# Performance work log

Hardware: AMD Instinct MI355X
Metric: run time of the kernel (lower is better)

Reference implementation:

```python
import jax, jax.numpy as jnp
import numpy as np

N_NODES = 100000
N_EDGES = 1600000
D_FEAT = 64
ORDER = 2


def setup_inputs() -> dict:
    key = jax.random.key(0)
    k1, k2, k3, k4 = jax.random.split(key, 4)
    x = jax.random.normal(k1, (N_NODES, D_FEAT), dtype=jnp.float32)
    edge_row = jnp.sort(jax.random.randint(k2, (N_EDGES,), 0, N_NODES, dtype=jnp.int32))
    edge_col = jax.random.randint(k3, (N_EDGES,), 0, N_NODES, dtype=jnp.int32)
    # positive edge weights ~ normalized adjacency values
    edge_val = jax.random.uniform(k4, (N_EDGES,), dtype=jnp.float32)
    return {"x": x, "edge_row": edge_row, "edge_col": edge_col, "edge_val": edge_val}


def reference(x, edge_row, edge_col, edge_val):
    # SGConvolution: x <- adj @ x, repeated `order` times (no trainable params).
    # adj is sparse COO: adj[edge_row[e], edge_col[e]] = edge_val[e].
    def spmm(h):
        # gather source features, scale by edge weight, scatter-add to rows
        msg = edge_val[:, None] * h[edge_col]          # [E, D]
        return jax.ops.segment_sum(msg, edge_row, num_segments=N_NODES)  # [N, D]

    h = x
    for _ in range(ORDER):
        h = spmm(h)
    return h
```

## Files before the change

### kernel.cpp

```cpp
#include <hip/hip_runtime.h>
#include <hip/hip_fp16.h>


#define N_NODES 100000
#define N_EDGES 1600000
#define D_FEAT  64
#define EPW     64
#define CH      16

#define N_ELEM   (N_NODES * D_FEAT)
#define N_CAST   (N_ELEM / 4)
#define N_Z16    (N_ELEM / 8)
#define N_ZOUT   (N_ELEM / 4)
#define PREP_TASKS (N_CAST + N_Z16 + N_ZOUT)

__device__ __forceinline__ float readlane_f(float x, int j) {
    return __uint_as_float(__builtin_amdgcn_readlane(__float_as_uint(x), j));
}

template <bool HALF_OUT>
__device__ __forceinline__ void flush(void* outp, int row, int lane, float acc) {
    if constexpr (HALF_OUT) {
        const float partner = __shfl_xor(acc, 1);
        if ((lane & 1) == 0) {
            __half2* o = (__half2*)outp;
            unsafeAtomicAdd(&o[(size_t)row * (D_FEAT / 2) + (lane >> 1)],
                            __floats2half2_rn(acc, partner));
        }
    } else {
        atomicAdd(&((float*)outp)[(size_t)row * D_FEAT + lane], acc);
    }
}

template <bool HALF_OUT>
__global__ __launch_bounds__(256) void sg_spmm(
    const __half* __restrict__ h,
    const int*    __restrict__ erow,
    const int*    __restrict__ ecol,
    const float*  __restrict__ eval,
    void*         __restrict__ outp)
{
    const int lane  = threadIdx.x & 63;
    const int wave  = (int)((blockIdx.x * blockDim.x + threadIdx.x) >> 6);
    const int start = wave * EPW;

    const int   r_v = erow[start + lane];
    const int   c_v = ecol[start + lane];
    const float w_v = eval[start + lane];

    __half gbuf[2][CH];

#pragma unroll
    for (int j = 0; j < CH; ++j) {
        const int c = __builtin_amdgcn_readlane(c_v, j);
        gbuf[0][j] = h[(size_t)c * D_FEAT + lane];
    }

    int   cur_row = __builtin_amdgcn_readlane(r_v, 0);
    float acc     = 0.0f;

#pragma unroll
    for (int k = 0; k < EPW / CH; ++k) {
        if (k + 1 < EPW / CH) {
#pragma unroll
            for (int j = 0; j < CH; ++j) {
                const int c = __builtin_amdgcn_readlane(c_v, (k + 1) * CH + j);
                gbuf[(k + 1) & 1][j] = h[(size_t)c * D_FEAT + lane];
            }
        }
#pragma unroll
        for (int j = 0; j < CH; ++j) {
            const int e = k * CH + j;
            const int r = __builtin_amdgcn_readlane(r_v, e);
            if (r != cur_row) {
                flush<HALF_OUT>(outp, cur_row, lane, acc);
                acc = 0.0f;
                cur_row = r;
            }
            acc += readlane_f(w_v, e) * __half2float(gbuf[k & 1][j]);
        }
    }
    flush<HALF_OUT>(outp, cur_row, lane, acc);
}

__global__ __launch_bounds__(256) void prep(
    const float* __restrict__ x,
    __half*      __restrict__ h16a,
    __half*      __restrict__ h16b,
    float*       __restrict__ out)
{
    const int i = blockIdx.x * blockDim.x + threadIdx.x;
    if (i < N_CAST) {
        const float4 v = ((const float4*)x)[i];
        const __half2 a = __floats2half2_rn(v.x, v.y);
        const __half2 b = __floats2half2_rn(v.z, v.w);
        uint2 u;
        u.x = *(const unsigned int*)&a;
        u.y = *(const unsigned int*)&b;
        ((uint2*)h16a)[i] = u;
    } else if (i < N_CAST + N_Z16) {
        ((uint4*)h16b)[i - N_CAST] = make_uint4(0u, 0u, 0u, 0u);
    } else {
        ((float4*)out)[i - (N_CAST + N_Z16)] = make_float4(0.f, 0.f, 0.f, 0.f);
    }
}

extern "C" void kernel_launch(void* const* d_in, const int* in_sizes, int n_in,
                              void* d_out, int out_size, void* d_ws, size_t ws_size,
                              hipStream_t stream) {
    const float* x    = (const float*)d_in[0];
    const int*   erow = (const int*)  d_in[1];
    const int*   ecol = (const int*)  d_in[2];
    const float* eval = (const float*)d_in[3];
    float*       out  = (float*)d_out;

    __half* h16a = (__half*)d_ws;
    __half* h16b = h16a + N_ELEM;

    const int threads     = 256;
    const int prep_blocks = PREP_TASKS / threads;
    const int spmm_blocks = (N_EDGES / EPW) * 64 / threads;

    prep<<<prep_blocks, threads, 0, stream>>>(x, h16a, h16b, out);
    sg_spmm<true ><<<spmm_blocks, threads, 0, stream>>>(h16a, erow, ecol, eval, h16b);
    sg_spmm<false><<<spmm_blocks, threads, 0, stream>>>(h16b, erow, ecol, eval, out);
}
```

Baseline: 153.9 us.

## Split each wave into half-waves that gather half2 rows over 32 edges

The SpMM kernel now splits each 64-lane wave into two 32-lane halves. Each half processes 32 of the wave's edges, and each lane loads a 4-byte half2 (two features) per edge instead of a single 2-byte half. Edge indices, rows and weights are broadcast with ds_bpermute instead of readlane, and all 32 gathers are issued up front rather than in double-buffered chunks of 16. This is meant to halve the load count per lane, widen each access and expose more memory-level parallelism. In exchange it costs more registers, a now-divergent per-half flush branch, and extra shuffles to re-order the fp32 output atomics.

After: 157.9 us. 1.03x slower.

```diff
diff --git a/kernel.cpp b/kernel.cpp
--- a/kernel.cpp
+++ b/kernel.cpp
@@ -6,7 +6,6 @@
 #define N_EDGES 1600000
 #define D_FEAT  64
 #define EPW     64
-#define CH      16
 
 #define N_ELEM   (N_NODES * D_FEAT)
 #define N_CAST   (N_ELEM / 4)
@@ -14,22 +13,35 @@
 #define N_ZOUT   (N_ELEM / 4)
 #define PREP_TASKS (N_CAST + N_Z16 + N_ZOUT)
 
-__device__ __forceinline__ float readlane_f(float x, int j) {
-    return __uint_as_float(__builtin_amdgcn_readlane(__float_as_uint(x), j));
+__device__ __forceinline__ int bperm(int baddr, int off, int v) {
+    return __builtin_amdgcn_ds_bpermute(baddr + off, v);
+}
+
+__device__ __forceinline__ void flush_f32(float* o, int row, int lane,
+                                          float ax, float ay) {
+    const int m = lane & 31;
+    const int H = lane & 32;
+    const float sx = __shfl(ax, H + (m >> 1));
+    const float sy = __shfl(ay, H + (m >> 1));
+    const float tx = __shfl(ax, H + 16 + (m >> 1));
+    const float ty = __shfl(ay, H + 16 + (m >> 1));
+    const float vA = (m & 1) ? sy : sx;
+    const float vB = (m & 1) ? ty : tx;
+    atomicAdd(&o[(size_t)row * D_FEAT + m], vA);
+    atomicAdd(&o[(size_t)row * D_FEAT + 32 + m], vB);
 }
 
 template <bool HALF_OUT>
-__device__ __forceinline__ void flush(void* outp, int row, int lane, float acc) {
+__device__ __forceinline__ void flush(void* outp, int row, int lane,
+                                      float& ax, float& ay) {
     if constexpr (HALF_OUT) {
-        const float partner = __shfl_xor(acc, 1);
-        if ((lane & 1) == 0) {
-            __half2* o = (__half2*)outp;
-            unsafeAtomicAdd(&o[(size_t)row * (D_FEAT / 2) + (lane >> 1)],
-                            __floats2half2_rn(acc, partner));
-        }
+        __half2* o = (__half2*)outp;
+        unsafeAtomicAdd(&o[(size_t)row * (D_FEAT / 2) + (lane & 31)],
+                        __floats2half2_rn(ax, ay));
     } else {
-        atomicAdd(&((float*)outp)[(size_t)row * D_FEAT + lane], acc);
+        flush_f32((float*)outp, row, lane, ax, ay);
     }
+    ax = 0.f; ay = 0.f;
 }
 
 template <bool HALF_OUT>
@@ -43,44 +55,37 @@
     const int lane  = threadIdx.x & 63;
     const int wave  = (int)((blockIdx.x * blockDim.x + threadIdx.x) >> 6);
     const int start = wave * EPW;
+    const int m     = lane & 31;
+    const int baddr = (lane & 32) * 4;
 
     const int   r_v = erow[start + lane];
     const int   c_v = ecol[start + lane];
     const float w_v = eval[start + lane];
 
-    __half gbuf[2][CH];
+    uint g[32];
+#pragma unroll
+    for (int p = 0; p < 32; ++p) {
+        const int cc = bperm(baddr, 4 * p, c_v);
+        g[p] = *((const uint*)(h + (size_t)cc * D_FEAT) + m);
+    }
+
+    int   cur_r = bperm(baddr, 0, r_v);
+    float ax = 0.f, ay = 0.f;
 
 #pragma unroll
-    for (int j = 0; j < CH; ++j) {
-        const int c = __builtin_amdgcn_readlane(c_v, j);
-        gbuf[0][j] = h[(size_t)c * D_FEAT + lane];
+    for (int p = 0; p < 32; ++p) {
+        const int rn = bperm(baddr, 4 * p, r_v);
+        if (rn != cur_r) {
+            flush<HALF_OUT>(outp, cur_r, lane, ax, ay);
+            cur_r = rn;
+        }
+        const float ww = __uint_as_float(
+            (unsigned)bperm(baddr, 4 * p, (int)__float_as_uint(w_v)));
+        const float2 f = __half22float2(__builtin_bit_cast(__half2, g[p]));
+        ax = fmaf(ww, f.x, ax);
+        ay = fmaf(ww, f.y, ay);
     }
-
-    int   cur_row = __builtin_amdgcn_readlane(r_v, 0);
-    float acc     = 0.0f;
-
-#pragma unroll
-    for (int k = 0; k < EPW / CH; ++k) {
-        if (k + 1 < EPW / CH) {
-#pragma unroll
-            for (int j = 0; j < CH; ++j) {
-                const int c = __builtin_amdgcn_readlane(c_v, (k + 1) * CH + j);
-                gbuf[(k + 1) & 1][j] = h[(size_t)c * D_FEAT + lane];
-            }
-        }
-#pragma unroll
-        for (int j = 0; j < CH; ++j) {
-            const int e = k * CH + j;
-            const int r = __builtin_amdgcn_readlane(r_v, e);
-            if (r != cur_row) {
-                flush<HALF_OUT>(outp, cur_row, lane, acc);
-                acc = 0.0f;
-                cur_row = r;
-            }
-            acc += readlane_f(w_v, e) * __half2float(gbuf[k & 1][j]);
-        }
-    }
-    flush<HALF_OUT>(outp, cur_row, lane, acc);
+    flush<HALF_OUT>(outp, cur_r, lane, ax, ay);
 }
 
 __global__ __launch_bounds__(256) void prep(
@@ -95,8 +100,8 @@
         const __half2 a = __floats2half2_rn(v.x, v.y);
         const __half2 b = __floats2half2_rn(v.z, v.w);
         uint2 u;
-        u.x = *(const unsigned int*)&a;
-        u.y = *(const unsigned int*)&b;
+        u.x = __builtin_bit_cast(unsigned int, a);
+        u.y = __builtin_bit_cast(unsigned int, b);
         ((uint2*)h16a)[i] = u;
     } else if (i < N_CAST + N_Z16) {
         ((uint4*)h16b)[i - N_CAST] = make_uint4(0u, 0u, 0u, 0u);
```
